# Kernel tuning notes

Measured on AMD Instinct MI355X. Metric: run time of the kernel, lower is better.

The kernel has to match this reference:

```python
import jax, jax.numpy as jnp
import numpy as np
import math

B, H, S, D = 2, 16, 2048, 64
NUM_BUCKETS = 32
MAX_DISTANCE = 128
TEMPERATURE = 8.0  # sqrt(D)
MASK_FILL = -1.0e9


def _relative_position_bucket(relative_position, num_buckets=NUM_BUCKETS, max_distance=MAX_DISTANCE):
    # bidirectional=True branch of the torch code
    num_buckets = num_buckets // 2
    n = -relative_position
    ret = (n < 0).astype(jnp.int32) * num_buckets
    n = jnp.abs(n)
    max_exact = num_buckets // 2
    is_small = n < max_exact
    val_if_large = max_exact + (
        jnp.log(n.astype(jnp.float32) / max_exact)
        / math.log(max_distance / max_exact)
        * (num_buckets - max_exact)
    ).astype(jnp.int32)
    val_if_large = jnp.minimum(val_if_large, num_buckets - 1)
    ret = ret + jnp.where(is_small, n, val_if_large)
    return ret


def setup_inputs() -> dict:
    key = jax.random.key(0)
    kq, kk, kv, kw, km = jax.random.split(key, 5)
    q = jax.random.normal(kq, (B, H, S, D), jnp.float32)
    k = jax.random.normal(kk, (B, H, S, D), jnp.float32)
    v = jax.random.normal(kv, (B, H, S, D), jnp.float32)
    bias_weight = jax.random.normal(kw, (NUM_BUCKETS, H), jnp.float32) * 0.02
    pos = jnp.broadcast_to(jnp.arange(S, dtype=jnp.int32)[None, :], (B, S))
    context_position = pos
    memory_position = pos
    mask = jax.random.randint(km, (B, 1, S, S), 0, 2) > 0  # bool, True = masked out
    return {
        'q': q, 'k': k, 'v': v, 'bias_weight': bias_weight,
        'context_position': context_position, 'memory_position': memory_position,
        'mask': mask,
    }


def reference(q, k, v, bias_weight, context_position, memory_position, mask):
    # attn scores: [B,H,S,S]
    attn = jnp.einsum('bhqd,bhkd->bhqk', q / TEMPERATURE, k)
    # T5-style relative position bias
    relative_position = memory_position[:, None, :] - context_position[:, :, None]  # [B,S,S]
    rp_bucket = _relative_position_bucket(relative_position)
    position_bias = bias_weight[rp_bucket]             # [B,S,S,H]
    position_bias = jnp.transpose(position_bias, (0, 3, 1, 2))  # [B,H,S,S]
    attn = attn + position_bias
    attn = jnp.where(mask, MASK_FILL, attn)
    attn = jax.nn.softmax(attn, axis=-1)  # dropout p=0.0 (eval) -> identity
    output = jnp.einsum('bhqk,bhkd->bhqd', attn, v)
    return output, attn, position_bias
```

## Files before the change

### kernel.cpp

```cpp
#include <hip/hip_runtime.h>
#include <math.h>

#define BB 2
#define HH 16
#define SS 2048
#define DD 64
#define TQ 8
#define STRIDE 2052

typedef __attribute__((ext_vector_type(8))) short bf16x8;
typedef __attribute__((ext_vector_type(4))) float f32x4;
typedef __attribute__((ext_vector_type(4))) int i32x4;

__device__ __forceinline__ unsigned short f2bf(float f) {
    unsigned u = __float_as_uint(f);
    u += 0x7FFF + ((u >> 16) & 1);
    return (unsigned short)(u >> 16);
}

__device__ __forceinline__ int rel_bucket(int cpq, int mpk) {
    int n = cpq - mpk;
    int ret = 0;
    if (n < 0) { ret = 16; n = -n; }
    int v;
    if (n < 8) v = n;
    else {
        int j = (n >= 12) + (n >= 16) + (n >= 23) + (n >= 32) +
                (n >= 46) + (n >= 64) + (n >= 91);
        v = 8 + j;
    }
    return ret + v;
}

__launch_bounds__(256)
__global__ void conv_k_bf16(const float* __restrict__ src,
                            unsigned short* __restrict__ dst) {
    const size_t i = ((size_t)blockIdx.x * 256 + threadIdx.x) * 8;
    float4 f0 = *(const float4*)(src + i);
    float4 f1 = *(const float4*)(src + i + 4);
    union { bf16x8 v; unsigned short u[8]; } o;
    o.u[0] = f2bf(f0.x); o.u[1] = f2bf(f0.y); o.u[2] = f2bf(f0.z); o.u[3] = f2bf(f0.w);
    o.u[4] = f2bf(f1.x); o.u[5] = f2bf(f1.y); o.u[6] = f2bf(f1.z); o.u[7] = f2bf(f1.w);
    *(bf16x8*)(dst + i) = o.v;
}

__launch_bounds__(512, 4)
__global__ void attn_tile_kernel(const float* __restrict__ qg,
                                 const unsigned short* __restrict__ kb,
                                 const float* __restrict__ vg,
                                 const float* __restrict__ bw,
                                 const int*   __restrict__ cp,
                                 const int*   __restrict__ mp,
                                 const int*   __restrict__ mask,
                                 float* __restrict__ o_out,
                                 float* __restrict__ a_out,
                                 float* __restrict__ p_out) {
    __shared__ __align__(16) float strip[TQ * STRIDE];
    __shared__ __align__(16) float partials[4 * TQ * DD];
    __shared__ __align__(16) unsigned short q_lds[16 * 72];
    __shared__ float bwh[32];
    __shared__ float invl[TQ];

    const int tid = threadIdx.x;
    const int x   = blockIdx.x;
    const int xcd = x & 7;
    const int s_  = x >> 3;
    const int bh  = xcd * 4 + (s_ & 3);
    const int qt  = s_ >> 2;
    const int b   = bh >> 4;
    const int h   = bh & 15;
    const int q0  = qt * TQ;

    const unsigned short* Kbase = kb + (size_t)bh * SS * DD;
    const float* Vbase = vg + (size_t)bh * SS * DD;

    {
        const float* Qrow = qg + ((size_t)bh * SS + q0) * DD;
        for (int e = tid; e < 16 * DD; e += 512) {
            int r = e >> 6, d = e & 63;
            q_lds[r * 72 + d] = (r < TQ) ? f2bf(Qrow[r * DD + d] * 0.125f)
                                         : (unsigned short)0;
        }
        if (tid < 32) bwh[tid] = bw[tid * HH + h];
    }
    __syncthreads();

    const int lane = tid & 63;
    const int wave = tid >> 6;
    const int quad = lane >> 4;
    const int l16  = lane & 15;

    {
        bf16x8 a0 = *(const bf16x8*)&q_lds[l16 * 72 + quad * 8];
        bf16x8 a1 = *(const bf16x8*)&q_lds[l16 * 72 + 32 + quad * 8];
        for (int ii = 0; ii < 16; ++ii) {
            const int kt = wave * 16 + ii;
            const unsigned short* kp = Kbase + (size_t)(kt * 16 + l16) * DD + quad * 8;
            bf16x8 b0 = *(const bf16x8*)(kp);
            bf16x8 b1 = *(const bf16x8*)(kp + 32);
            f32x4 acc = {0.f, 0.f, 0.f, 0.f};
            acc = __builtin_amdgcn_mfma_f32_16x16x32_bf16(a0, b0, acc, 0, 0, 0);
            acc = __builtin_amdgcn_mfma_f32_16x16x32_bf16(a1, b1, acc, 0, 0, 0);
            if (quad < 2) {
                const int col = kt * 16 + l16;
                const int rb  = quad * 4;
                strip[(rb + 0) * STRIDE + col] = acc[0];
                strip[(rb + 1) * STRIDE + col] = acc[1];
                strip[(rb + 2) * STRIDE + col] = acc[2];
                strip[(rb + 3) * STRIDE + col] = acc[3];
            }
        }
    }
    __syncthreads();

    {
        const int r  = wave;
        const int i  = lane;
        const int qi = q0 + r;
        const int cpq = cp[b * SS + qi];
        const int* mrow = mask + ((size_t)b * SS + qi) * SS;
        const int* mpb  = mp + b * SS;
        float* prow = p_out + ((size_t)bh * SS + qi) * SS;
        float* srow = strip + r * STRIDE;
        float mx = -3.0e38f;
        for (int j = 0; j < 8; ++j) {
            const int c0 = (i + 64 * j) * 4;
            i32x4 m4  = *(const i32x4*)(mrow + c0);
            i32x4 mp4 = *(const i32x4*)(mpb + c0);
            f32x4 s4  = *(const f32x4*)(srow + c0);
            f32x4 p4, sv;
            #pragma unroll
            for (int u = 0; u < 4; ++u) {
                p4[u] = bwh[rel_bucket(cpq, mp4[u])];
                float s = s4[u] + p4[u];
                if (m4[u] != 0) s = -1.0e9f;
                sv[u] = s;
                mx = fmaxf(mx, s);
            }
            *(f32x4*)(srow + c0) = sv;
            *(f32x4*)(prow + c0) = p4;
        }
        #pragma unroll
        for (int off = 32; off >= 1; off >>= 1)
            mx = fmaxf(mx, __shfl_xor(mx, off));
        float sum = 0.f;
        for (int j = 0; j < 8; ++j) {
            const int c0 = (i + 64 * j) * 4;
            f32x4 s4 = *(const f32x4*)(srow + c0);
            f32x4 e4;
            #pragma unroll
            for (int u = 0; u < 4; ++u) {
                e4[u] = __expf(s4[u] - mx);
                sum += e4[u];
            }
            *(f32x4*)(srow + c0) = e4;
        }
        #pragma unroll
        for (int off = 32; off >= 1; off >>= 1)
            sum += __shfl_xor(sum, off);
        if (i == 0) invl[r] = 1.0f / sum;
    }
    __syncthreads();

    {
        float* abase = a_out + ((size_t)bh * SS + q0) * SS;
        #pragma unroll
        for (int r = 0; r < TQ; ++r) {
            const float iv = invl[r];
            f32x4 s4 = *(const f32x4*)&strip[r * STRIDE + tid * 4];
            f32x4 o4;
            o4[0] = s4[0] * iv; o4[1] = s4[1] * iv;
            o4[2] = s4[2] * iv; o4[3] = s4[3] * iv;
            *(f32x4*)(abase + (size_t)r * SS + tid * 4) = o4;
        }
    }

    {
        const int kc = wave & 3;
        const int rb = (wave >> 2) * 4;
        const int d  = lane;
        float acc0 = 0.f, acc1 = 0.f, acc2 = 0.f, acc3 = 0.f;
        const int cbeg = kc * 512;
        for (int c0 = cbeg; c0 < cbeg + 512; c0 += 4) {
            f32x4 e0 = *(const f32x4*)&strip[(rb + 0) * STRIDE + c0];
            f32x4 e1 = *(const f32x4*)&strip[(rb + 1) * STRIDE + c0];
            f32x4 e2 = *(const f32x4*)&strip[(rb + 2) * STRIDE + c0];
            f32x4 e3 = *(const f32x4*)&strip[(rb + 3) * STRIDE + c0];
            #pragma unroll
            for (int u = 0; u < 4; ++u) {
                const float vv = Vbase[(size_t)(c0 + u) * DD + d];
                acc0 += e0[u] * vv;
                acc1 += e1[u] * vv;
                acc2 += e2[u] * vv;
                acc3 += e3[u] * vv;
            }
        }
        partials[kc * (TQ * DD) + (rb + 0) * DD + d] = acc0;
        partials[kc * (TQ * DD) + (rb + 1) * DD + d] = acc1;
        partials[kc * (TQ * DD) + (rb + 2) * DD + d] = acc2;
        partials[kc * (TQ * DD) + (rb + 3) * DD + d] = acc3;
    }
    __syncthreads();

    {
        const int r = tid >> 6;
        const float v = partials[tid] + partials[512 + tid] +
                        partials[1024 + tid] + partials[1536 + tid];
        o_out[((size_t)bh * SS + q0 + r) * DD + (tid & 63)] = v * invl[r];
    }
}

extern "C" void kernel_launch(void* const* d_in, const int* in_sizes, int n_in,
                              void* d_out, int out_size, void* d_ws, size_t ws_size,
                              hipStream_t stream) {
    const float* q  = (const float*)d_in[0];
    const float* k  = (const float*)d_in[1];
    const float* v  = (const float*)d_in[2];
    const float* bw = (const float*)d_in[3];
    const int*   cp = (const int*)d_in[4];
    const int*   mp = (const int*)d_in[5];
    const int*   mask = (const int*)d_in[6];

    float* o_out = (float*)d_out;
    float* a_out = o_out + (size_t)BB * HH * SS * DD;
    float* p_out = a_out + (size_t)BB * HH * SS * SS;

    unsigned short* kb = (unsigned short*)d_ws;
    const int conv_grid = (BB * HH * SS * DD) / (8 * 256);
    conv_k_bf16<<<conv_grid, 256, 0, stream>>>(k, kb);

    const int grid = BB * HH * (SS / TQ);
    attn_tile_kernel<<<grid, 512, 0, stream>>>(q, kb, v, bw, cp, mp, mask,
                                               o_out, a_out, p_out);
}
```

Measured before the change: 1.653 ms.

## Compute PV product with split-bf16 MFMA on pre-transposed V

```diff
diff --git a/kernel.cpp b/kernel.cpp
--- a/kernel.cpp
+++ b/kernel.cpp
@@ -6,16 +6,22 @@
 #define SS 2048
 #define DD 64
 #define TQ 8
-#define STRIDE 2052
+#define FSTRIDE 2052
+#define ERS 2056
+#define ELO (8 * ERS)
 
 typedef __attribute__((ext_vector_type(8))) short bf16x8;
 typedef __attribute__((ext_vector_type(4))) float f32x4;
 typedef __attribute__((ext_vector_type(4))) int i32x4;
+typedef __attribute__((ext_vector_type(4))) unsigned short u16x4;
 
 __device__ __forceinline__ unsigned short f2bf(float f) {
     unsigned u = __float_as_uint(f);
     u += 0x7FFF + ((u >> 16) & 1);
     return (unsigned short)(u >> 16);
+}
+__device__ __forceinline__ float bf2f(unsigned short h) {
+    return __uint_as_float(((unsigned)h) << 16);
 }
 
 __device__ __forceinline__ int rel_bucket(int cpq, int mpk) {
@@ -44,10 +50,40 @@
     *(bf16x8*)(dst + i) = o.v;
 }
 
+__launch_bounds__(256)
+__global__ void conv_v_t(const float* __restrict__ v,
+                         unsigned short* __restrict__ vt_hi,
+                         unsigned short* __restrict__ vt_lo) {
+    __shared__ float tile[64][65];
+    const int bh = blockIdx.x >> 5;
+    const int ct = blockIdx.x & 31;
+    const int c0 = ct * 64;
+    const float* vb = v + ((size_t)bh * SS + c0) * DD;
+    const int tid = threadIdx.x;
+    #pragma unroll
+    for (int it = 0; it < 16; ++it) {
+        const int idx = it * 256 + tid;
+        tile[idx >> 6][idx & 63] = vb[idx];
+    }
+    __syncthreads();
+    #pragma unroll
+    for (int it = 0; it < 16; ++it) {
+        const int idx = it * 256 + tid;
+        const int d = idx >> 6, c = idx & 63;
+        const float val = tile[c][d];
+        const unsigned short hi = f2bf(val);
+        const unsigned short lo = f2bf(val - bf2f(hi));
+        const size_t o = ((size_t)bh * DD + d) * SS + c0 + c;
+        vt_hi[o] = hi;
+        vt_lo[o] = lo;
+    }
+}
+
 __launch_bounds__(512, 4)
 __global__ void attn_tile_kernel(const float* __restrict__ qg,
                                  const unsigned short* __restrict__ kb,
-                                 const float* __restrict__ vg,
+                                 const unsigned short* __restrict__ vt_hi,
+                                 const unsigned short* __restrict__ vt_lo,
                                  const float* __restrict__ bw,
                                  const int*   __restrict__ cp,
                                  const int*   __restrict__ mp,
@@ -55,11 +91,12 @@
                                  float* __restrict__ o_out,
                                  float* __restrict__ a_out,
                                  float* __restrict__ p_out) {
-    __shared__ __align__(16) float strip[TQ * STRIDE];
-    __shared__ __align__(16) float partials[4 * TQ * DD];
+    __shared__ __align__(16) unsigned short strip_sh[2 * 8 * ERS];
+    __shared__ __align__(16) float partials[2 * TQ * DD];
     __shared__ __align__(16) unsigned short q_lds[16 * 72];
     __shared__ float bwh[32];
     __shared__ float invl[TQ];
+    float* strip = (float*)strip_sh;
 
     const int tid = threadIdx.x;
     const int x   = blockIdx.x;
@@ -72,7 +109,6 @@
     const int q0  = qt * TQ;
 
     const unsigned short* Kbase = kb + (size_t)bh * SS * DD;
-    const float* Vbase = vg + (size_t)bh * SS * DD;
 
     {
         const float* Qrow = qg + ((size_t)bh * SS + q0) * DD;
@@ -104,10 +140,10 @@
             if (quad < 2) {
                 const int col = kt * 16 + l16;
                 const int rb  = quad * 4;
-                strip[(rb + 0) * STRIDE + col] = acc[0];
-                strip[(rb + 1) * STRIDE + col] = acc[1];
-                strip[(rb + 2) * STRIDE + col] = acc[2];
-                strip[(rb + 3) * STRIDE + col] = acc[3];
+                strip[(rb + 0) * FSTRIDE + col] = acc[0];
+                strip[(rb + 1) * FSTRIDE + col] = acc[1];
+                strip[(rb + 2) * FSTRIDE + col] = acc[2];
+                strip[(rb + 3) * FSTRIDE + col] = acc[3];
             }
         }
     }
@@ -121,91 +157,102 @@
         const int* mrow = mask + ((size_t)b * SS + qi) * SS;
         const int* mpb  = mp + b * SS;
         float* prow = p_out + ((size_t)bh * SS + qi) * SS;
-        float* srow = strip + r * STRIDE;
+        const float* srow = strip + r * FSTRIDE;
+        float sv[32];
         float mx = -3.0e38f;
+        #pragma unroll
         for (int j = 0; j < 8; ++j) {
             const int c0 = (i + 64 * j) * 4;
             i32x4 m4  = *(const i32x4*)(mrow + c0);
             i32x4 mp4 = *(const i32x4*)(mpb + c0);
             f32x4 s4  = *(const f32x4*)(srow + c0);
-            f32x4 p4, sv;
+            f32x4 p4;
             #pragma unroll
             for (int u = 0; u < 4; ++u) {
                 p4[u] = bwh[rel_bucket(cpq, mp4[u])];
                 float s = s4[u] + p4[u];
                 if (m4[u] != 0) s = -1.0e9f;
-                sv[u] = s;
+                sv[j * 4 + u] = s;
                 mx = fmaxf(mx, s);
             }
-            *(f32x4*)(srow + c0) = sv;
             *(f32x4*)(prow + c0) = p4;
         }
         #pragma unroll
         for (int off = 32; off >= 1; off >>= 1)
             mx = fmaxf(mx, __shfl_xor(mx, off));
+
+        __syncthreads();
+
         float sum = 0.f;
+        #pragma unroll
+        for (int j = 0; j < 32; ++j) {
+            sv[j] = __expf(sv[j] - mx);
+            sum += sv[j];
+        }
+        #pragma unroll
+        for (int off = 32; off >= 1; off >>= 1)
+            sum += __shfl_xor(sum, off);
+        const float inv = 1.0f / sum;
+        if (i == 0) invl[r] = inv;
+
+        unsigned short* ehr = strip_sh + r * ERS;
+        unsigned short* elr = strip_sh + ELO + r * ERS;
+        float* arow = a_out + ((size_t)bh * SS + qi) * SS;
+        #pragma unroll
         for (int j = 0; j < 8; ++j) {
             const int c0 = (i + 64 * j) * 4;
-            f32x4 s4 = *(const f32x4*)(srow + c0);
-            f32x4 e4;
+            f32x4 o4;
+            u16x4 h4, l4;
             #pragma unroll
             for (int u = 0; u < 4; ++u) {
-                e4[u] = __expf(s4[u] - mx);
-                sum += e4[u];
-            }
-            *(f32x4*)(srow + c0) = e4;
-        }
-        #pragma unroll
-        for (int off = 32; off >= 1; off >>= 1)
-            sum += __shfl_xor(sum, off);
-        if (i == 0) invl[r] = 1.0f / sum;
-    }
-    __syncthreads();
-
-    {
-        float* abase = a_out + ((size_t)bh * SS + q0) * SS;
-        #pragma unroll
-        for (int r = 0; r < TQ; ++r) {
-            const float iv = invl[r];
-            f32x4 s4 = *(const f32x4*)&strip[r * STRIDE + tid * 4];
-            f32x4 o4;
-            o4[0] = s4[0] * iv; o4[1] = s4[1] * iv;
-            o4[2] = s4[2] * iv; o4[3] = s4[3] * iv;
-            *(f32x4*)(abase + (size_t)r * SS + tid * 4) = o4;
-        }
-    }
-
-    {
-        const int kc = wave & 3;
-        const int rb = (wave >> 2) * 4;
-        const int d  = lane;
-        float acc0 = 0.f, acc1 = 0.f, acc2 = 0.f, acc3 = 0.f;
-        const int cbeg = kc * 512;
-        for (int c0 = cbeg; c0 < cbeg + 512; c0 += 4) {
-            f32x4 e0 = *(const f32x4*)&strip[(rb + 0) * STRIDE + c0];
-            f32x4 e1 = *(const f32x4*)&strip[(rb + 1) * STRIDE + c0];
-            f32x4 e2 = *(const f32x4*)&strip[(rb + 2) * STRIDE + c0];
-            f32x4 e3 = *(const f32x4*)&strip[(rb + 3) * STRIDE + c0];
+                const float e = sv[j * 4 + u];
+                o4[u] = e * inv;
+                const unsigned short hi = f2bf(e);
+                h4[u] = hi;
+                l4[u] = f2bf(e - bf2f(hi));
+            }
+            *(f32x4*)(arow + c0) = o4;
+            *(u16x4*)(ehr + c0) = h4;
+            *(u16x4*)(elr + c0) = l4;
+        }
+    }
+    __syncthreads();
+
+    {
+        const int kc = wave >> 2;
+        const int d0 = (wave & 3) * 16;
+        const unsigned short* vhiB = vt_hi + ((size_t)bh * DD + d0 + l16) * SS;
+        const unsigned short* vloB = vt_lo + ((size_t)bh * DD + d0 + l16) * SS;
+        const unsigned short* ehB = strip_sh + (l16 & 7) * ERS + quad * 8;
+        const unsigned short* elB = strip_sh + ELO + (l16 & 7) * ERS + quad * 8;
+        f32x4 acc1 = {0.f, 0.f, 0.f, 0.f};
+        f32x4 acc2 = {0.f, 0.f, 0.f, 0.f};
+        f32x4 acc3 = {0.f, 0.f, 0.f, 0.f};
+        #pragma unroll 4
+        for (int s = 0; s < 32; ++s) {
+            const int k0 = kc * 1024 + s * 32;
+            bf16x8 ahi = *(const bf16x8*)(ehB + k0);
+            bf16x8 alo = *(const bf16x8*)(elB + k0);
+            bf16x8 bhi = *(const bf16x8*)(vhiB + k0 + quad * 8);
+            bf16x8 blo = *(const bf16x8*)(vloB + k0 + quad * 8);
+            acc1 = __builtin_amdgcn_mfma_f32_16x16x32_bf16(ahi, bhi, acc1, 0, 0, 0);
+            acc2 = __builtin_amdgcn_mfma_f32_16x16x32_bf16(alo, bhi, acc2, 0, 0, 0);
+            acc3 = __builtin_amdgcn_mfma_f32_16x16x32_bf16(ahi, blo, acc3, 0, 0, 0);
+        }
+        if (quad < 2) {
             #pragma unroll
-            for (int u = 0; u < 4; ++u) {
-                const float vv = Vbase[(size_t)(c0 + u) * DD + d];
-                acc0 += e0[u] * vv;
-                acc1 += e1[u] * vv;
-                acc2 += e2[u] * vv;
-                acc3 += e3[u] * vv;
-            }
-        }
-        partials[kc * (TQ * DD) + (rb + 0) * DD + d] = acc0;
-        partials[kc * (TQ * DD) + (rb + 1) * DD + d] = acc1;
-        partials[kc * (TQ * DD) + (rb + 2) * DD + d] = acc2;
-        partials[kc * (TQ * DD) + (rb + 3) * DD + d] = acc3;
+            for (int rg = 0; rg < 4; ++rg) {
+                const int row = quad * 4 + rg;
+                partials[kc * (TQ * DD) + row * DD + d0 + l16] =
+                    acc1[rg] + acc2[rg] + acc3[rg];
+            }
+        }
     }
     __syncthreads();
 
     {
         const int r = tid >> 6;
-        const float v = partials[tid] + partials[512 + tid] +
-                        partials[1024 + tid] + partials[1536 + tid];
+        const float v = partials[tid] + partials[512 + tid];
         o_out[((size_t)bh * SS + q0 + r) * DD + (tid & 63)] = v * invl[r];
     }
 }
@@ -225,11 +272,16 @@
     float* a_out = o_out + (size_t)BB * HH * SS * DD;
     float* p_out = a_out + (size_t)BB * HH * SS * SS;
 
-    unsigned short* kb = (unsigned short*)d_ws;
-    const int conv_grid = (BB * HH * SS * DD) / (8 * 256);
+    const size_t NE = (size_t)BB * HH * SS * DD;
+    unsigned short* kb    = (unsigned short*)d_ws;
+    unsigned short* vt_hi = kb + NE;
+    unsigned short* vt_lo = kb + 2 * NE;
+
+    const int conv_grid = (int)(NE / (8 * 256));
     conv_k_bf16<<<conv_grid, 256, 0, stream>>>(k, kb);
+    conv_v_t<<<BB * HH * (SS / 64), 256, 0, stream>>>(v, vt_hi, vt_lo);
 
     const int grid = BB * HH * (SS / TQ);
-    attn_tile_kernel<<<grid, 512, 0, stream>>>(q, kb, v, bw, cp, mp, mask,
+    attn_tile_kernel<<<grid, 512, 0, stream>>>(q, kb, vt_hi, vt_lo, bw, cp, mp, mask,
                                                o_out, a_out, p_out);
 }
```

After: 1.772 ms. 1.07x slower.
